# Kernel optimization log

Hardware: AMD Instinct MI355X
Metric: run time of the kernel (lower is better)

The kernel has to match this reference:

```python
import jax, jax.numpy as jnp
import numpy as np

EPS = 1e-4  # ridge term added to W W^T before inversion


def setup_inputs() -> dict:
    key = jax.random.key(0)
    k1, k2 = jax.random.split(key)
    B, F, C, D = 4096, 2048, 100, 16
    x = jax.random.normal(k1, (B, F), dtype=jnp.float32)
    # match torch reset_parameters: uniform(-stdv, stdv), stdv = 1/sqrt(F)
    stdv = 1.0 / np.sqrt(F)
    weight = jax.random.uniform(k2, (C, D, F), dtype=jnp.float32, minval=-stdv, maxval=stdv)
    return {"x": x, "weight": weight}


def reference(x, weight):
    # weight: [C, D, F], x: [B, F]
    C, D, F = weight.shape
    # per-capsule Gram matrix W W^T : [C, D, D]
    weight_caps = jnp.einsum('cdf,cef->cde', weight, weight)
    sigma = jnp.linalg.inv(weight_caps + EPS * jnp.eye(D, dtype=weight.dtype))
    # u[b,c,d] = <x_b, W_{c,d}>  (the x @ W^T projection of the original)
    u = jnp.einsum('bf,cdf->bcd', x, weight)
    # original chain: (u @ sigma @ W) @ x == u^T sigma u  (same math, no [B,C,F] temp)
    out = jnp.einsum('bcd,cde,bce->bc', u, sigma, u)
    return jnp.sqrt(out)
```

## Files before the change

### kernel.cpp

```cpp
#include <hip/hip_runtime.h>
#include <hip/hip_bf16.h>
#include <math.h>

#define F_DIM 2048
#define B_DIM 4096
#define C_DIM 100
#define D_DIM 16
#define N_DIM (C_DIM*D_DIM)
#define N_PAD 1664
#define RIDGE_EPS 1e-4f

typedef __attribute__((ext_vector_type(8))) short bf16x8;
typedef __attribute__((ext_vector_type(4))) float f32x4;

__device__ __forceinline__ void gload16(const void* g, void* l) {
  __builtin_amdgcn_global_load_lds(
      (const __attribute__((address_space(1))) void*)g,
      (__attribute__((address_space(3))) void*)l,
      16, 0, 0);
}

#define VM_BAR(N) asm volatile("s_waitcnt vmcnt(" #N ")\n\ts_barrier" ::: "memory")
#define LGKM_BAR() asm volatile("s_waitcnt lgkmcnt(0)\n\ts_barrier" ::: "memory")

__device__ __forceinline__ unsigned short f2bf(float f) {
  unsigned u = __float_as_uint(f);
  u += 0x7FFFu + ((u >> 16) & 1u);
  return (unsigned short)(u >> 16);
}

__global__ __launch_bounds__(256) void cvt_gram_kernel(
    const float* __restrict__ x, const float* __restrict__ w,
    unsigned short* __restrict__ xb, unsigned short* __restrict__ wb,
    float* __restrict__ sigma, int nx8, int nw8, int npad8) {
  __shared__ float part[4][64][4];
  __shared__ float G[16][17];
  __shared__ float IV[16][17];
  int t = threadIdx.x;
  if (blockIdx.x < C_DIM) {
    int c = blockIdx.x;
    int lane = t & 63, wid = t >> 6;
    const float* src = w + (size_t)c * (D_DIM * F_DIM)
                         + (size_t)(lane & 15) * F_DIM + ((lane >> 4) * 8) + wid * 512;
    f32x4 g = {0.f, 0.f, 0.f, 0.f};
#pragma unroll
    for (int kt = 0; kt < 16; ++kt) {
      float4 v0 = *(const float4*)(src + kt * 32);
      float4 v1 = *(const float4*)(src + kt * 32 + 4);
      bf16x8 f;
      f[0] = (short)f2bf(v0.x); f[1] = (short)f2bf(v0.y);
      f[2] = (short)f2bf(v0.z); f[3] = (short)f2bf(v0.w);
      f[4] = (short)f2bf(v1.x); f[5] = (short)f2bf(v1.y);
      f[6] = (short)f2bf(v1.z); f[7] = (short)f2bf(v1.w);
      g = __builtin_amdgcn_mfma_f32_16x16x32_bf16(f, f, g, 0, 0, 0);
    }
#pragma unroll
    for (int j = 0; j < 4; j++) part[wid][lane][j] = g[j];
    int d = t >> 4, e = t & 15;
    IV[d][e] = (d == e) ? 1.f : 0.f;
    __syncthreads();
    if (t < 64) {
      int col = t & 15;
#pragma unroll
      for (int j = 0; j < 4; j++) {
        int row = (t >> 4) * 4 + j;
        float s4 = part[0][t][j] + part[1][t][j] + part[2][t][j] + part[3][t][j];
        G[row][col] = s4 + (row == col ? RIDGE_EPS : 0.f);
      }
    }
    __syncthreads();
    for (int k = 0; k < 16; k++) {
      float piv = G[k][k];
      float gke = G[k][e];
      float ike = IV[k][e];
      float f   = G[d][k];
      float gde = G[d][e];
      float ide = IV[d][e];
      __syncthreads();
      if (d == k) {
        G[k][e]  = gke / piv;
        IV[k][e] = ike / piv;
      } else {
        G[d][e]  = gde - f * gke / piv;
        IV[d][e] = ide - f * ike / piv;
      }
      __syncthreads();
    }
    sigma[(size_t)c * 256 + t] = IV[d][e];
    return;
  }
  int i = (blockIdx.x - C_DIM) * 256 + t;
  const float* in; unsigned short* outp; int idx;
  if (i < nx8) { in = x; outp = xb; idx = i; }
  else {
    idx = i - nx8;
    if (idx >= nw8) {
      int idx3 = idx - nw8;
      if (idx3 < npad8) {
        uint4 z = {0, 0, 0, 0};
        *((uint4*)(wb + (size_t)N_DIM * F_DIM) + idx3) = z;
      }
      return;
    }
    in = w; outp = wb;
  }
  const float4* p = (const float4*)in + (size_t)idx * 2;
  float4 a = p[0], b = p[1];
  float v[8] = {a.x, a.y, a.z, a.w, b.x, b.y, b.z, b.w};
  union { unsigned short u16[8]; uint4 u4; } r;
#pragma unroll
  for (int j = 0; j < 8; j++) r.u16[j] = f2bf(v[j]);
  *((uint4*)outp + idx) = r.u4;
}

__global__ __launch_bounds__(256) void gemm_caps_kernel(
    const unsigned short* __restrict__ xb,
    const unsigned short* __restrict__ wb,
    const float* __restrict__ sigma,
    float* __restrict__ out)
{
  __shared__ __align__(16) unsigned char smem[65536];
  const int t = threadIdx.x;
  const int lane = t & 63;
  const int wid = t >> 6;
  const int wr = wid >> 1, wc = wid & 1;
  const int bid = blockIdx.x;
  const int swz = (bid & 7) * 52 + (bid >> 3);
  const int bn = swz % 13;
  const int bm = swz / 13;
  const int rowBase = bm * 128;
  const int colBase = bn * 128;

  unsigned char* buf0 = smem;
  unsigned char* buf1 = smem + 32768;

  const unsigned short* srcA[4]; unsigned qA[4];
  const unsigned short* srcB[4]; unsigned qB[4];
#pragma unroll
  for (int i = 0; i < 4; i++) {
    unsigned q = (unsigned)wid * 4096u + (unsigned)i * 1024u + (unsigned)lane * 16u;
    unsigned r = q >> 7, b = q & 127u;
    unsigned cb = b ^ ((r & 7u) << 4);
    qA[i] = q;
    srcA[i] = xb + (size_t)(rowBase + (int)r) * F_DIM + (cb >> 1);
    qB[i] = 16384u + q;
    srcB[i] = wb + (size_t)(colBase + (int)r) * F_DIM + (cb >> 1);
  }

  int aOff[4][2], bOff[4][2];
#pragma unroll
  for (int m = 0; m < 4; m++) {
    int r = wr * 64 + m * 16 + (lane & 15);
    int sw = (r & 7) << 4;
#pragma unroll
    for (int ks = 0; ks < 2; ks++) {
      int kb = ks * 64 + ((lane >> 4) << 4);
      aOff[m][ks] = r * 128 + (kb ^ sw);
    }
  }
#pragma unroll
  for (int n = 0; n < 4; n++) {
    int r = wc * 64 + n * 16 + (lane & 15);
    int sw = (r & 7) << 4;
#pragma unroll
    for (int ks = 0; ks < 2; ks++) {
      int kb = ks * 64 + ((lane >> 4) << 4);
      bOff[n][ks] = 16384 + r * 128 + (kb ^ sw);
    }
  }

  f32x4 acc[4][4];
#pragma unroll
  for (int m = 0; m < 4; m++)
#pragma unroll
    for (int n = 0; n < 4; n++)
      acc[m][n] = (f32x4){0.f, 0.f, 0.f, 0.f};

  auto stage = [&](unsigned char* buf, int kt) {
    const size_t koff = (size_t)kt * 64;
#pragma unroll
    for (int i = 0; i < 4; i++) gload16(srcA[i] + koff, buf + qA[i]);
#pragma unroll
    for (int i = 0; i < 4; i++) gload16(srcB[i] + koff, buf + qB[i]);
  };
  auto compute = [&](const unsigned char* buf) {
#pragma unroll
    for (int ks = 0; ks < 2; ks++) {
      bf16x8 a0 = *(const bf16x8*)(buf + aOff[0][ks]);
      bf16x8 a1 = *(const bf16x8*)(buf + aOff[1][ks]);
      bf16x8 a2 = *(const bf16x8*)(buf + aOff[2][ks]);
      bf16x8 a3 = *(const bf16x8*)(buf + aOff[3][ks]);
      bf16x8 b0 = *(const bf16x8*)(buf + bOff[0][ks]);
      bf16x8 b1 = *(const bf16x8*)(buf + bOff[1][ks]);
      bf16x8 b2 = *(const bf16x8*)(buf + bOff[2][ks]);
      bf16x8 b3 = *(const bf16x8*)(buf + bOff[3][ks]);
      __builtin_amdgcn_s_setprio(1);
      acc[0][0] = __builtin_amdgcn_mfma_f32_16x16x32_bf16(a0, b0, acc[0][0], 0, 0, 0);
      acc[0][1] = __builtin_amdgcn_mfma_f32_16x16x32_bf16(a0, b1, acc[0][1], 0, 0, 0);
      acc[0][2] = __builtin_amdgcn_mfma_f32_16x16x32_bf16(a0, b2, acc[0][2], 0, 0, 0);
      acc[0][3] = __builtin_amdgcn_mfma_f32_16x16x32_bf16(a0, b3, acc[0][3], 0, 0, 0);
      acc[1][0] = __builtin_amdgcn_mfma_f32_16x16x32_bf16(a1, b0, acc[1][0], 0, 0, 0);
      acc[1][1] = __builtin_amdgcn_mfma_f32_16x16x32_bf16(a1, b1, acc[1][1], 0, 0, 0);
      acc[1][2] = __builtin_amdgcn_mfma_f32_16x16x32_bf16(a1, b2, acc[1][2], 0, 0, 0);
      acc[1][3] = __builtin_amdgcn_mfma_f32_16x16x32_bf16(a1, b3, acc[1][3], 0, 0, 0);
      acc[2][0] = __builtin_amdgcn_mfma_f32_16x16x32_bf16(a2, b0, acc[2][0], 0, 0, 0);
      acc[2][1] = __builtin_amdgcn_mfma_f32_16x16x32_bf16(a2, b1, acc[2][1], 0, 0, 0);
      acc[2][2] = __builtin_amdgcn_mfma_f32_16x16x32_bf16(a2, b2, acc[2][2], 0, 0, 0);
      acc[2][3] = __builtin_amdgcn_mfma_f32_16x16x32_bf16(a2, b3, acc[2][3], 0, 0, 0);
      acc[3][0] = __builtin_amdgcn_mfma_f32_16x16x32_bf16(a3, b0, acc[3][0], 0, 0, 0);
      acc[3][1] = __builtin_amdgcn_mfma_f32_16x16x32_bf16(a3, b1, acc[3][1], 0, 0, 0);
      acc[3][2] = __builtin_amdgcn_mfma_f32_16x16x32_bf16(a3, b2, acc[3][2], 0, 0, 0);
      acc[3][3] = __builtin_amdgcn_mfma_f32_16x16x32_bf16(a3, b3, acc[3][3], 0, 0, 0);
      __builtin_amdgcn_s_setprio(0);
    }
  };

  stage(buf0, 0);
  for (int kt = 0; kt < 30; kt += 2) {
    stage(buf1, kt + 1);
    VM_BAR(8);
    compute(buf0);
    LGKM_BAR();
    stage(buf0, kt + 2);
    VM_BAR(8);
    compute(buf1);
    LGKM_BAR();
  }
  stage(buf1, 31);
  VM_BAR(8);
  compute(buf0);
  LGKM_BAR();
  VM_BAR(0);
  compute(buf1);
  LGKM_BAR();

  float* uT = (float*)smem;
#pragma unroll
  for (int m = 0; m < 4; m++)
#pragma unroll
    for (int n = 0; n < 4; n++)
#pragma unroll
      for (int j = 0; j < 4; j++) {
        int row = wr * 64 + m * 16 + ((lane >> 4) << 2) + j;
        int col = wc * 64 + n * 16 + (lane & 15);
        int g = (col >> 2) ^ ((row & 7) << 2);
        uT[row * 128 + g * 4 + (col & 3)] = acc[m][n][j];
      }
  __syncthreads();
  const int capBase = bn * 8;
#pragma unroll
  for (int pp = 0; pp < 4; ++pp) {
    int pi = t + pp * 256;
    int row = pi & 127;
    int cl = __builtin_amdgcn_readfirstlane(pi >> 7);
    float ur[16];
#pragma unroll
    for (int q = 0; q < 4; q++) {
      int g = (cl * 4 + q) ^ ((row & 7) << 2);
      f32x4 v = *(const f32x4*)(uT + row * 128 + g * 4);
#pragma unroll
      for (int j = 0; j < 4; j++) ur[q * 4 + j] = v[j];
    }
    int cap = capBase + cl;
    const float* s = sigma + (size_t)cap * 256;
    float qf = 0.f;
#pragma unroll
    for (int dd = 0; dd < 16; ++dd) {
      float td = 0.f;
#pragma unroll
      for (int ee = 0; ee < 16; ++ee) td = fmaf(s[dd * 16 + ee], ur[ee], td);
      qf = fmaf(ur[dd], td, qf);
    }
    if (cap < C_DIM)
      out[(size_t)(rowBase + row) * C_DIM + cap] = sqrtf(fmaxf(qf, 0.f));
  }
}

extern "C" void kernel_launch(void* const* d_in, const int* in_sizes, int n_in,
                              void* d_out, int out_size, void* d_ws, size_t ws_size,
                              hipStream_t stream) {
  const float* x = (const float*)d_in[0];
  const float* w = (const float*)d_in[1];
  float* out = (float*)d_out;

  unsigned short* xb = (unsigned short*)d_ws;
  unsigned short* wb = xb + (size_t)B_DIM * F_DIM;
  float* sigma = (float*)(wb + (size_t)N_PAD * F_DIM);

  int nx8 = B_DIM * F_DIM / 8;
  int nw8 = N_DIM * F_DIM / 8;
  int npad8 = (N_PAD - N_DIM) * F_DIM / 8;
  int nconv = nx8 + nw8 + npad8;
  int grid = C_DIM + (nconv + 255) / 256;
  cvt_gram_kernel<<<grid, 256, 0, stream>>>(x, w, xb, wb, sigma, nx8, nw8, npad8);
  gemm_caps_kernel<<<(B_DIM / 128) * (N_PAD / 128), 256, 0, stream>>>(xb, wb, sigma, out);
}
```

Before: 56.81 us.

## Fuse x fp32-to-bf16 conversion into GEMM A-tile load path

Drops the separate pass that converts x to bf16 in the prep kernel. The GEMM now loads fp32 x tiles into registers, converts them to bf16 and writes them into swizzled LDS, while W still uses direct global-to-LDS loads. This saves writing and re-reading a 16 MB bf16 copy of x. In exchange, each x tile is re-read in fp32 by all 13 column blocks, conversion work moves into the GEMM loop, and full vmcnt(0) barriers replace the partial waits. The epilogue LDS swizzle is also changed to reduce bank conflicts.

```diff
diff --git a/kernel.cpp b/kernel.cpp
--- a/kernel.cpp
+++ b/kernel.cpp
@@ -12,6 +12,7 @@
 
 typedef __attribute__((ext_vector_type(8))) short bf16x8;
 typedef __attribute__((ext_vector_type(4))) float f32x4;
+typedef __attribute__((ext_vector_type(2))) unsigned int u32x2;
 
 __device__ __forceinline__ void gload16(const void* g, void* l) {
   __builtin_amdgcn_global_load_lds(
@@ -20,8 +21,7 @@
       16, 0, 0);
 }
 
-#define VM_BAR(N) asm volatile("s_waitcnt vmcnt(" #N ")\n\ts_barrier" ::: "memory")
-#define LGKM_BAR() asm volatile("s_waitcnt lgkmcnt(0)\n\ts_barrier" ::: "memory")
+#define FULL_BAR() asm volatile("s_waitcnt vmcnt(0) lgkmcnt(0)\n\ts_barrier" ::: "memory")
 
 __device__ __forceinline__ unsigned short f2bf(float f) {
   unsigned u = __float_as_uint(f);
@@ -30,9 +30,8 @@
 }
 
 __global__ __launch_bounds__(256) void cvt_gram_kernel(
-    const float* __restrict__ x, const float* __restrict__ w,
-    unsigned short* __restrict__ xb, unsigned short* __restrict__ wb,
-    float* __restrict__ sigma, int nx8, int nw8, int npad8) {
+    const float* __restrict__ w, unsigned short* __restrict__ wb,
+    float* __restrict__ sigma, int nw8, int npad8) {
   __shared__ float part[4][64][4];
   __shared__ float G[16][17];
   __shared__ float IV[16][17];
@@ -89,32 +88,26 @@
     sigma[(size_t)c * 256 + t] = IV[d][e];
     return;
   }
-  int i = (blockIdx.x - C_DIM) * 256 + t;
-  const float* in; unsigned short* outp; int idx;
-  if (i < nx8) { in = x; outp = xb; idx = i; }
-  else {
-    idx = i - nx8;
-    if (idx >= nw8) {
-      int idx3 = idx - nw8;
-      if (idx3 < npad8) {
-        uint4 z = {0, 0, 0, 0};
-        *((uint4*)(wb + (size_t)N_DIM * F_DIM) + idx3) = z;
-      }
-      return;
-    }
-    in = w; outp = wb;
-  }
-  const float4* p = (const float4*)in + (size_t)idx * 2;
+  int idx = (blockIdx.x - C_DIM) * 256 + t;
+  if (idx >= nw8) {
+    int idx3 = idx - nw8;
+    if (idx3 < npad8) {
+      uint4 z = {0, 0, 0, 0};
+      *((uint4*)(wb + (size_t)N_DIM * F_DIM) + idx3) = z;
+    }
+    return;
+  }
+  const float4* p = (const float4*)w + (size_t)idx * 2;
   float4 a = p[0], b = p[1];
   float v[8] = {a.x, a.y, a.z, a.w, b.x, b.y, b.z, b.w};
   union { unsigned short u16[8]; uint4 u4; } r;
 #pragma unroll
   for (int j = 0; j < 8; j++) r.u16[j] = f2bf(v[j]);
-  *((uint4*)outp + idx) = r.u4;
+  *((uint4*)wb + idx) = r.u4;
 }
 
 __global__ __launch_bounds__(256) void gemm_caps_kernel(
-    const unsigned short* __restrict__ xb,
+    const float* __restrict__ x,
     const unsigned short* __restrict__ wb,
     const float* __restrict__ sigma,
     float* __restrict__ out)
@@ -134,15 +127,19 @@
   unsigned char* buf0 = smem;
   unsigned char* buf1 = smem + 32768;
 
-  const unsigned short* srcA[4]; unsigned qA[4];
+  const float* aSrc = x + (size_t)(rowBase + wid * 32 + (lane >> 4)) * F_DIM + (lane & 15) * 4;
+  int wOffA[8];
+#pragma unroll
+  for (int i = 0; i < 8; i++) {
+    int r = wid * 32 + i * 4 + (lane >> 4);
+    wOffA[i] = r * 128 + (((lane & 15) * 8) ^ ((r & 7) << 4));
+  }
   const unsigned short* srcB[4]; unsigned qB[4];
 #pragma unroll
   for (int i = 0; i < 4; i++) {
     unsigned q = (unsigned)wid * 4096u + (unsigned)i * 1024u + (unsigned)lane * 16u;
     unsigned r = q >> 7, b = q & 127u;
     unsigned cb = b ^ ((r & 7u) << 4);
-    qA[i] = q;
-    srcA[i] = xb + (size_t)(rowBase + (int)r) * F_DIM + (cb >> 1);
     qB[i] = 16384u + q;
     srcB[i] = wb + (size_t)(colBase + (int)r) * F_DIM + (cb >> 1);
   }
@@ -176,12 +173,25 @@
     for (int n = 0; n < 4; n++)
       acc[m][n] = (f32x4){0.f, 0.f, 0.f, 0.f};
 
-  auto stage = [&](unsigned char* buf, int kt) {
+  f32x4 areg[8];
+  auto loadA = [&](int kt) {
+#pragma unroll
+    for (int i = 0; i < 8; i++)
+      areg[i] = *(const f32x4*)(aSrc + (size_t)i * 4 * F_DIM + kt * 64);
+  };
+  auto loadB = [&](unsigned char* buf, int kt) {
     const size_t koff = (size_t)kt * 64;
 #pragma unroll
-    for (int i = 0; i < 4; i++) gload16(srcA[i] + koff, buf + qA[i]);
-#pragma unroll
     for (int i = 0; i < 4; i++) gload16(srcB[i] + koff, buf + qB[i]);
+  };
+  auto writeA = [&](unsigned char* buf) {
+#pragma unroll
+    for (int i = 0; i < 8; i++) {
+      unsigned lo = ((unsigned)f2bf(areg[i][1]) << 16) | f2bf(areg[i][0]);
+      unsigned hi = ((unsigned)f2bf(areg[i][3]) << 16) | f2bf(areg[i][2]);
+      u32x2 v; v[0] = lo; v[1] = hi;
+      *(u32x2*)(buf + wOffA[i]) = v;
+    }
   };
   auto compute = [&](const unsigned char* buf) {
 #pragma unroll
@@ -215,24 +225,32 @@
     }
   };
 
-  stage(buf0, 0);
+  loadA(0);
+  loadB(buf0, 0);
+  writeA(buf0);
+  FULL_BAR();
   for (int kt = 0; kt < 30; kt += 2) {
-    stage(buf1, kt + 1);
-    VM_BAR(8);
+    loadA(kt + 1);
+    loadB(buf1, kt + 1);
     compute(buf0);
-    LGKM_BAR();
-    stage(buf0, kt + 2);
-    VM_BAR(8);
+    __builtin_amdgcn_sched_barrier(0);
+    writeA(buf1);
+    FULL_BAR();
+    loadA(kt + 2);
+    loadB(buf0, kt + 2);
     compute(buf1);
-    LGKM_BAR();
-  }
-  stage(buf1, 31);
-  VM_BAR(8);
+    __builtin_amdgcn_sched_barrier(0);
+    writeA(buf0);
+    FULL_BAR();
+  }
+  loadA(31);
+  loadB(buf1, 31);
   compute(buf0);
-  LGKM_BAR();
-  VM_BAR(0);
+  __builtin_amdgcn_sched_barrier(0);
+  writeA(buf1);
+  FULL_BAR();
   compute(buf1);
-  LGKM_BAR();
+  asm volatile("s_waitcnt lgkmcnt(0)\n\ts_barrier" ::: "memory");
 
   float* uT = (float*)smem;
 #pragma unroll
@@ -243,7 +261,7 @@
       for (int j = 0; j < 4; j++) {
         int row = wr * 64 + m * 16 + ((lane >> 4) << 2) + j;
         int col = wc * 64 + n * 16 + (lane & 15);
-        int g = (col >> 2) ^ ((row & 7) << 2);
+        int g = (col >> 2) ^ (row & 3) ^ ((row >> 2) & 7);
         uT[row * 128 + g * 4 + (col & 3)] = acc[m][n][j];
       }
   __syncthreads();
@@ -256,7 +274,7 @@
     float ur[16];
 #pragma unroll
     for (int q = 0; q < 4; q++) {
-      int g = (cl * 4 + q) ^ ((row & 7) << 2);
+      int g = (cl * 4 + q) ^ (row & 3) ^ ((row >> 2) & 7);
       f32x4 v = *(const f32x4*)(uT + row * 128 + g * 4);
 #pragma unroll
       for (int j = 0; j < 4; j++) ur[q * 4 + j] = v[j];
@@ -283,15 +301,12 @@
   const float* w = (const float*)d_in[1];
   float* out = (float*)d_out;
 
-  unsigned short* xb = (unsigned short*)d_ws;
-  unsigned short* wb = xb + (size_t)B_DIM * F_DIM;
+  unsigned short* wb = (unsigned short*)d_ws;
   float* sigma = (float*)(wb + (size_t)N_PAD * F_DIM);
 
-  int nx8 = B_DIM * F_DIM / 8;
   int nw8 = N_DIM * F_DIM / 8;
   int npad8 = (N_PAD - N_DIM) * F_DIM / 8;
-  int nconv = nx8 + nw8 + npad8;
-  int grid = C_DIM + (nconv + 255) / 256;
-  cvt_gram_kernel<<<grid, 256, 0, stream>>>(x, w, xb, wb, sigma, nx8, nw8, npad8);
-  gemm_caps_kernel<<<(B_DIM / 128) * (N_PAD / 128), 256, 0, stream>>>(xb, wb, sigma, out);
-}
+  int grid = C_DIM + (nw8 + npad8 + 255) / 256;
+  cvt_gram_kernel<<<grid, 256, 0, stream>>>(w, wb, sigma, nw8, npad8);
+  gemm_caps_kernel<<<(B_DIM / 128) * (N_PAD / 128), 256, 0, stream>>>(x, wb, sigma, out);
+}
```

Result: slower. 66.71 us (+17.4%).
